# Performance work log

Hardware: AMD Instinct MI355X
Metric: run time of the kernel (lower is better)

Reference implementation:

```python
import jax, jax.numpy as jnp
import numpy as np

D_MODEL = 1024
NUM_HEADS = 16
D_HEAD = D_MODEL // NUM_HEADS
B, S = 4, 2048


def setup_inputs() -> dict:
    key = jax.random.key(0)
    ks = jax.random.split(key, 11)
    s = 1.0 / np.sqrt(D_MODEL)
    inp = {
        "query": jax.random.normal(ks[0], (B, S, D_MODEL), jnp.float32),
        "key": jax.random.normal(ks[1], (B, S, D_MODEL), jnp.float32),
        "value": jax.random.normal(ks[2], (B, S, D_MODEL), jnp.float32),
        "Wq": jax.random.uniform(ks[3], (D_MODEL, D_MODEL), jnp.float32, -s, s),
        "bq": jax.random.uniform(ks[4], (D_MODEL,), jnp.float32, -s, s),
        "Wk": jax.random.uniform(ks[5], (D_MODEL, D_MODEL), jnp.float32, -s, s),
        "bk": jax.random.uniform(ks[6], (D_MODEL,), jnp.float32, -s, s),
        "Wv": jax.random.uniform(ks[7], (D_MODEL, D_MODEL), jnp.float32, -s, s),
        "bv": jax.random.uniform(ks[8], (D_MODEL,), jnp.float32, -s, s),
        "Wo": jax.random.uniform(ks[9], (D_MODEL, D_MODEL), jnp.float32, -s, s),
        "bo": jax.random.uniform(ks[10], (D_MODEL,), jnp.float32, -s, s),
    }
    return inp


def reference(query, key, value, Wq, bq, Wk, bk, Wv, bv, Wo, bo):
    # Linear projections (torch Linear: x @ W.T + b)
    q = query @ Wq.T + bq  # [B,S,D]
    k = key @ Wk.T + bk
    v = value @ Wv.T + bv
    # split heads -> [B,H,S,Dh]
    def split(x):
        return x.reshape(B, S, NUM_HEADS, D_HEAD).transpose(0, 2, 1, 3)
    q, k, v = split(q), split(k), split(v)
    scale = 1.0 / np.sqrt(D_HEAD).astype(np.float32)
    scores = jnp.einsum('bhqd,bhkd->bhqk', q, k) * scale
    attn = jax.nn.softmax(scores, axis=-1)  # dropout is identity in eval
    ctx = jnp.einsum('bhqk,bhkd->bhqd', attn, v)
    ctx = ctx.transpose(0, 2, 1, 3).reshape(B, S, D_MODEL)
    return ctx @ Wo.T + bo
```

## Files before the change

kernel.cpp:

```cpp
#include <hip/hip_runtime.h>
#include <hip/hip_bf16.h>

typedef __bf16 bf16;
typedef bf16 bf16x8 __attribute__((ext_vector_type(8)));
typedef float f32x4 __attribute__((ext_vector_type(4)));
typedef float f32x16 __attribute__((ext_vector_type(16)));
typedef unsigned int u32x2 __attribute__((ext_vector_type(2)));
typedef unsigned int u32x4 __attribute__((ext_vector_type(4)));

#define B_  4
#define S_  2048
#define DM  1024
#define NH  16
#define DH  64

#define QSCALE 0.18033688011112042f


__device__ __forceinline__ void async_copy16(const void* g, void* lds) {
    __builtin_amdgcn_global_load_lds(
        (const __attribute__((address_space(1))) void*)g,
        (__attribute__((address_space(3))) void*)lds,
        16, 0, 0);
}

__device__ __forceinline__ bf16x8 read_frag(const char* lds, int row, int kbyte) {
    int off = row * 128 + (kbyte ^ ((row & 7) << 4));
    return *(const bf16x8*)(lds + off);
}

template<int ROWS>
__device__ __forceinline__ void stage_g2l(const bf16* g, int gs, char* lds) {
    int t = threadIdx.x;
#pragma unroll
    for (int i = 0; i < ROWS * 8 / 256; ++i) {
        int c = i * 256 + t;
        int r = c >> 3;
        int s = (c & 7) ^ (r & 7);
        async_copy16(g + r * gs + s * 8, lds + c * 16);
    }
}

__device__ __forceinline__ unsigned cvt_pk(float lo, float hi) {
    unsigned r;
    asm("v_cvt_pk_bf16_f32 %0, %1, %2" : "=v"(r) : "v"(lo), "v"(hi));
    return r;
}

__device__ __forceinline__ u32x2 pl32swap(unsigned a, unsigned b) {
    return __builtin_amdgcn_permlane32_swap(a, b, false, false);
}


__device__ __forceinline__ void cvt_body(const float* __restrict__ s, bf16* __restrict__ d, int n8) {
    for (int i = blockIdx.x * 256 + threadIdx.x; i < n8; i += gridDim.x * 256) {
        f32x4 v0 = *(const f32x4*)(s + (long)i * 8);
        f32x4 v1 = *(const f32x4*)(s + (long)i * 8 + 4);
        bf16x8 r;
#pragma unroll
        for (int j = 0; j < 4; ++j) { r[j] = (bf16)v0[j]; r[j + 4] = (bf16)v1[j]; }
        *(bf16x8*)(d + (long)i * 8) = r;
    }
}

__global__ __launch_bounds__(256) void cvt_x(
    const float* __restrict__ a, const float* __restrict__ b, const float* __restrict__ c,
    bf16* __restrict__ oa, bf16* __restrict__ ob, bf16* __restrict__ oc)
{
    int z = blockIdx.y;
    cvt_body(z == 0 ? a : z == 1 ? b : c, z == 0 ? oa : z == 1 ? ob : oc, B_ * S_ * DM / 8);
}

__global__ __launch_bounds__(256) void cvt_w(
    const float* __restrict__ a, const float* __restrict__ b,
    const float* __restrict__ c, const float* __restrict__ d,
    bf16* __restrict__ oa, bf16* __restrict__ ob, bf16* __restrict__ oc, bf16* __restrict__ od)
{
    int z = blockIdx.y;
    cvt_body(z == 0 ? a : z == 1 ? b : z == 2 ? c : d,
             z == 0 ? oa : z == 1 ? ob : z == 2 ? oc : od, DM * DM / 8);
}


__device__ __forceinline__ void gemm_main(
    const bf16* __restrict__ A, const bf16* __restrict__ Wt,
    char* As, char* Bs, int m0, int n0, int lane, int wm, int wn, f32x4 (&acc)[4][4])
{
#pragma unroll
    for (int i = 0; i < 4; ++i)
#pragma unroll
        for (int j = 0; j < 4; ++j) acc[i][j] = f32x4{0.f, 0.f, 0.f, 0.f};

    for (int k0 = 0; k0 < DM; k0 += 64) {
        __syncthreads();
        stage_g2l<128>(A + (long)m0 * DM + k0, DM, As);
        stage_g2l<128>(Wt + (long)n0 * DM + k0, DM, Bs);
        __syncthreads();
#pragma unroll
        for (int ks = 0; ks < 2; ++ks) {
            int kb = ks * 64 + (lane >> 4) * 16;
            bf16x8 af[4], bfr[4];
#pragma unroll
            for (int f = 0; f < 4; ++f) af[f]  = read_frag(As, wm + f * 16 + (lane & 15), kb);
#pragma unroll
            for (int f = 0; f < 4; ++f) bfr[f] = read_frag(Bs, wn + f * 16 + (lane & 15), kb);
#pragma unroll
            for (int mf = 0; mf < 4; ++mf)
#pragma unroll
                for (int nf = 0; nf < 4; ++nf)
                    acc[mf][nf] = __builtin_amdgcn_mfma_f32_16x16x32_bf16(
                        af[mf], bfr[nf], acc[mf][nf], 0, 0, 0);
        }
    }
}

__global__ __launch_bounds__(256) void qkv_gemm(
    const bf16* __restrict__ xq, const bf16* __restrict__ xk, const bf16* __restrict__ xv,
    const bf16* __restrict__ wq, const bf16* __restrict__ wk, const bf16* __restrict__ wv,
    const float* __restrict__ bq, const float* __restrict__ bk, const float* __restrict__ bv,
    bf16* __restrict__ qo, bf16* __restrict__ ko, bf16* __restrict__ vo)
{
    __shared__ alignas(128) char As[128 * 128];
    __shared__ alignas(128) char Bs[128 * 128];

    int z = blockIdx.z;
    const bf16* X     = (z == 0) ? xq : (z == 1) ? xk : xv;
    const bf16* W     = (z == 0) ? wq : (z == 1) ? wk : wv;
    const float* bias = (z == 0) ? bq : (z == 1) ? bk : bv;
    bf16* out         = (z == 0) ? qo : (z == 1) ? ko : vo;
    float scale       = (z == 0) ? QSCALE : 1.0f;
    bool  vt          = (z == 2);

    int m0 = blockIdx.y * 128, n0 = blockIdx.x * 128;
    int lane = threadIdx.x & 63, wid = threadIdx.x >> 6;
    int wm = (wid >> 1) * 64, wn = (wid & 1) * 64;

    f32x4 acc[4][4];
    gemm_main(X, W, As, Bs, m0, n0, lane, wm, wn, acc);

#pragma unroll
    for (int nf = 0; nf < 4; ++nf) {
        int j = n0 + wn + nf * 16 + (lane & 15);
        float bj = bias[j];
        int h = j >> 6, dh = j & 63;
#pragma unroll
        for (int mf = 0; mf < 4; ++mf) {
#pragma unroll
            for (int r = 0; r < 4; ++r) {
                int i = m0 + wm + mf * 16 + (lane >> 4) * 4 + r;
                float v = (acc[mf][nf][r] + bj) * scale;
                int b = i >> 11, s = i & 2047;
                long addr = vt ? ((long)((b * NH + h) * DH + dh)) * S_ + s
                               : ((long)((b * NH + h) * S_ + s)) * DH + dh;
                out[addr] = (bf16)v;
            }
        }
    }
}

__global__ __launch_bounds__(256) void out_gemm(
    const bf16* __restrict__ ctxb, const bf16* __restrict__ wo, const float* __restrict__ bo,
    float* __restrict__ out)
{
    __shared__ alignas(128) char As[128 * 128];
    __shared__ alignas(128) char Bs[128 * 128];

    int m0 = blockIdx.y * 128, n0 = blockIdx.x * 128;
    int lane = threadIdx.x & 63, wid = threadIdx.x >> 6;
    int wm = (wid >> 1) * 64, wn = (wid & 1) * 64;

    f32x4 acc[4][4];
    gemm_main(ctxb, wo, As, Bs, m0, n0, lane, wm, wn, acc);

#pragma unroll
    for (int nf = 0; nf < 4; ++nf) {
        int j = n0 + wn + nf * 16 + (lane & 15);
        float bj = bo[j];
#pragma unroll
        for (int mf = 0; mf < 4; ++mf)
#pragma unroll
            for (int r = 0; r < 4; ++r) {
                int i = m0 + wm + mf * 16 + (lane >> 4) * 4 + r;
                out[(long)i * DM + j] = acc[mf][nf][r] + bj;
            }
    }
}

__global__ __launch_bounds__(256) void attn_fwd(
    const bf16* __restrict__ qb, const bf16* __restrict__ kb, const bf16* __restrict__ vtb,
    bf16* __restrict__ ctx)
{
    __shared__ alignas(128) char Ks[2][64 * 128];
    __shared__ alignas(128) char Vs[2][64 * 128];

    int bid = blockIdx.x;
    int xcd = bid & 7, rest = bid >> 3;
    int qt = rest & 15, bh = xcd + 8 * (rest >> 4);

    int lane = threadIdx.x & 63, wid = threadIdx.x >> 6;
    int ln = lane & 31, h = lane >> 5;
    int q0w = qt * 128 + wid * 32;

    const bf16* qg = qb + (long)bh * S_ * DH;
    const bf16* kg = kb + (long)bh * S_ * DH;
    const bf16* vg = vtb + (long)bh * DH * S_;

    bf16x8 qf[4];
#pragma unroll
    for (int s = 0; s < 4; ++s)
        qf[s] = *(const bf16x8*)(qg + (long)(q0w + ln) * DH + s * 16 + h * 8);

    const bf16x8 onea = __builtin_bit_cast(bf16x8,
        u32x4{0x3F803F80u, 0x3F803F80u, 0x3F803F80u, 0x3F803F80u});

    f32x16 o[2];
#pragma unroll
    for (int t = 0; t < 2; ++t)
#pragma unroll
        for (int r = 0; r < 16; ++r) o[t][r] = 0.f;
    f32x16 lacc;
#pragma unroll
    for (int r = 0; r < 16; ++r) lacc[r] = 0.f;

    stage_g2l<64>(kg, DH, Ks[0]);
    stage_g2l<64>(vg, S_, Vs[0]);
    __syncthreads();

    int cur = 0;
    for (int kt2 = 0; kt2 < S_ / 64; ++kt2) {
        f32x16 acc[2];
#pragma unroll
        for (int t = 0; t < 2; ++t)
#pragma unroll
            for (int r = 0; r < 16; ++r) acc[t][r] = 0.f;
        __builtin_amdgcn_s_setprio(1);
#pragma unroll
        for (int t = 0; t < 2; ++t)
#pragma unroll
            for (int s = 0; s < 4; ++s) {
                bf16x8 ka = read_frag(Ks[cur], 32 * t + ln, 32 * s + 16 * h);
                acc[t] = __builtin_amdgcn_mfma_f32_32x32x16_bf16(ka, qf[s], acc[t], 0, 0, 0);
            }
        __builtin_amdgcn_s_setprio(0);

        if (kt2 + 1 < S_ / 64) {
            stage_g2l<64>(kg + (long)(kt2 + 1) * 64 * DH, DH, Ks[cur ^ 1]);
            stage_g2l<64>(vg + (kt2 + 1) * 64, S_, Vs[cur ^ 1]);
        }

#pragma unroll
        for (int t = 0; t < 2; ++t)
#pragma unroll
            for (int r = 0; r < 16; ++r)
                acc[t][r] = __builtin_amdgcn_exp2f(acc[t][r]);

        unsigned pf[4][4];
#pragma unroll
        for (int t = 0; t < 2; ++t)
#pragma unroll
            for (int hf = 0; hf < 2; ++hf) {
                int rb = 8 * hf;
                unsigned a0 = cvt_pk(acc[t][rb + 0], acc[t][rb + 1]);
                unsigned s0 = cvt_pk(acc[t][rb + 4], acc[t][rb + 5]);
                unsigned a1 = cvt_pk(acc[t][rb + 2], acc[t][rb + 3]);
                unsigned s1 = cvt_pk(acc[t][rb + 6], acc[t][rb + 7]);
                u32x2 r0 = pl32swap(a0, s0);
                u32x2 r1 = pl32swap(a1, s1);
                int kt = 2 * t + hf;
                pf[kt][0] = r0.x; pf[kt][2] = r0.y;
                pf[kt][1] = r1.x; pf[kt][3] = r1.y;
            }

        __builtin_amdgcn_s_setprio(1);
#pragma unroll
        for (int kt = 0; kt < 4; ++kt) {
            bf16x8 pb = __builtin_bit_cast(bf16x8,
                u32x4{pf[kt][0], pf[kt][1], pf[kt][2], pf[kt][3]});
            bf16x8 va0 = read_frag(Vs[cur], ln,      32 * kt + 16 * h);
            o[0] = __builtin_amdgcn_mfma_f32_32x32x16_bf16(va0, pb, o[0], 0, 0, 0);
            bf16x8 va1 = read_frag(Vs[cur], 32 + ln, 32 * kt + 16 * h);
            o[1] = __builtin_amdgcn_mfma_f32_32x32x16_bf16(va1, pb, o[1], 0, 0, 0);
            lacc = __builtin_amdgcn_mfma_f32_32x32x16_bf16(onea, pb, lacc, 0, 0, 0);
        }
        __builtin_amdgcn_s_setprio(0);

        __syncthreads();
        cur ^= 1;
    }

    int b = bh >> 4, head = bh & 15;
    float inv = 1.0f / lacc[0];
    int s = q0w + ln;
    bf16* base = ctx + ((long)(b * S_ + s)) * DM + head * DH;
#pragma unroll
    for (int dt = 0; dt < 2; ++dt)
#pragma unroll
        for (int c = 0; c < 4; ++c) {
            int d0 = 32 * dt + 8 * c + 4 * h;
            u32x2 st;
            st.x = cvt_pk(o[dt][4 * c + 0] * inv, o[dt][4 * c + 1] * inv);
            st.y = cvt_pk(o[dt][4 * c + 2] * inv, o[dt][4 * c + 3] * inv);
            *(u32x2*)(base + d0) = st;
        }
}

extern "C" void kernel_launch(void* const* d_in, const int* in_sizes, int n_in,
                              void* d_out, int out_size, void* d_ws, size_t ws_size,
                              hipStream_t stream) {
    const float* query = (const float*)d_in[0];
    const float* key   = (const float*)d_in[1];
    const float* value = (const float*)d_in[2];
    const float* Wq = (const float*)d_in[3];
    const float* bq = (const float*)d_in[4];
    const float* Wk = (const float*)d_in[5];
    const float* bk = (const float*)d_in[6];
    const float* Wv = (const float*)d_in[7];
    const float* bv = (const float*)d_in[8];
    const float* Wo = (const float*)d_in[9];
    const float* bo = (const float*)d_in[10];
    float* out = (float*)d_out;

    char* ws = (char*)d_ws;
    const long MB = 1ll << 20;
    bf16* qb   = (bf16*)(ws + 0 * MB);
    bf16* kb   = (bf16*)(ws + 16 * MB);
    bf16* vtb  = (bf16*)(ws + 32 * MB);
    bf16* xqb  = (bf16*)(ws + 48 * MB);
    bf16* xkb  = (bf16*)(ws + 64 * MB);
    bf16* xvb  = (bf16*)(ws + 80 * MB);
    bf16* wqb  = (bf16*)(ws + 96 * MB);
    bf16* wkb  = (bf16*)(ws + 98 * MB);
    bf16* wvb  = (bf16*)(ws + 100 * MB);
    bf16* wob  = (bf16*)(ws + 102 * MB);
    bf16* ctxb = xqb;

    dim3 blk(256);
    cvt_x<<<dim3(2048, 3), blk, 0, stream>>>(query, key, value, xqb, xkb, xvb);
    cvt_w<<<dim3(512, 4), blk, 0, stream>>>(Wq, Wk, Wv, Wo, wqb, wkb, wvb, wob);
    qkv_gemm<<<dim3(8, 64, 3), blk, 0, stream>>>(xqb, xkb, xvb, wqb, wkb, wvb,
                                                 bq, bk, bv, qb, kb, vtb);
    attn_fwd<<<dim3(1024), blk, 0, stream>>>(qb, kb, vtb, ctxb);
    out_gemm<<<dim3(8, 64), blk, 0, stream>>>(ctxb, wob, bo, out);
}
```

Before: 237.5 us.

## Replace projection GEMMs with 256x256 8-wave pipelined double-buffered kernels

Rewrites the QKV and output projection GEMMs to use 256x256 tiles with 512 threads and 128KB of LDS. Global-to-LDS async loads for the next K slabs are interleaved with MFMA phases under explicit vmcnt waits and barriers. The aim is to hide load latency and raise data reuse per tile, replacing the previous sync-load-compute loop. In exchange the grid shrinks considerably (128 blocks for the output GEMM), which may leave CUs idle, and the large LDS footprint limits residency.

```diff
diff --git a/kernel.cpp b/kernel.cpp
--- a/kernel.cpp
+++ b/kernel.cpp
@@ -29,15 +29,15 @@
     return *(const bf16x8*)(lds + off);
 }
 
-template<int ROWS>
+template<int ROWS, int NT>
 __device__ __forceinline__ void stage_g2l(const bf16* g, int gs, char* lds) {
     int t = threadIdx.x;
 #pragma unroll
-    for (int i = 0; i < ROWS * 8 / 256; ++i) {
-        int c = i * 256 + t;
+    for (int i = 0; i < ROWS * 8 / NT; ++i) {
+        int c = i * NT + t;
         int r = c >> 3;
         int s = (c & 7) ^ (r & 7);
-        async_copy16(g + r * gs + s * 8, lds + c * 16);
+        async_copy16(g + (long)r * gs + s * 8, lds + c * 16);
     }
 }
 
@@ -82,46 +82,138 @@
 }
 
 
-__device__ __forceinline__ void gemm_main(
-    const bf16* __restrict__ A, const bf16* __restrict__ Wt,
-    char* As, char* Bs, int m0, int n0, int lane, int wm, int wn, f32x4 (&acc)[4][4])
-{
-#pragma unroll
-    for (int i = 0; i < 4; ++i)
-#pragma unroll
-        for (int j = 0; j < 4; ++j) acc[i][j] = f32x4{0.f, 0.f, 0.f, 0.f};
-
-    for (int k0 = 0; k0 < DM; k0 += 64) {
-        __syncthreads();
-        stage_g2l<128>(A + (long)m0 * DM + k0, DM, As);
-        stage_g2l<128>(Wt + (long)n0 * DM + k0, DM, Bs);
-        __syncthreads();
-#pragma unroll
-        for (int ks = 0; ks < 2; ++ks) {
-            int kb = ks * 64 + (lane >> 4) * 16;
-            bf16x8 af[4], bfr[4];
-#pragma unroll
-            for (int f = 0; f < 4; ++f) af[f]  = read_frag(As, wm + f * 16 + (lane & 15), kb);
-#pragma unroll
-            for (int f = 0; f < 4; ++f) bfr[f] = read_frag(Bs, wn + f * 16 + (lane & 15), kb);
+__device__ __forceinline__ void ph_read(const char* Ab, const char* Bb,
+        int qa, int qb, int wr, int wc, int lane,
+        bf16x8 (&af)[4][2], bf16x8 (&bfr)[2][2]) {
+#pragma unroll
+    for (int mf = 0; mf < 4; ++mf)
+#pragma unroll
+        for (int ks = 0; ks < 2; ++ks)
+            af[mf][ks] = read_frag(Ab, 128 * qa + 64 * wr + 16 * mf + (lane & 15),
+                                   ks * 64 + (lane >> 4) * 16);
+#pragma unroll
+    for (int nf = 0; nf < 2; ++nf)
+#pragma unroll
+        for (int ks = 0; ks < 2; ++ks)
+            bfr[nf][ks] = read_frag(Bb, 128 * qb + 32 * wc + 16 * nf + (lane & 15),
+                                    ks * 64 + (lane >> 4) * 16);
+}
+
+__device__ __forceinline__ void ph_mfma(bf16x8 (&af)[4][2], bf16x8 (&bfr)[2][2],
+                                        f32x4 (&acc)[4][2]) {
+    __builtin_amdgcn_s_barrier();
+    asm volatile("s_waitcnt lgkmcnt(0)" ::: "memory");
+    __builtin_amdgcn_sched_barrier(0);
+    __builtin_amdgcn_s_setprio(1);
+#pragma unroll
+    for (int mf = 0; mf < 4; ++mf)
+#pragma unroll
+        for (int nf = 0; nf < 2; ++nf)
+#pragma unroll
+            for (int ks = 0; ks < 2; ++ks)
+                acc[mf][nf] = __builtin_amdgcn_mfma_f32_16x16x32_bf16(
+                    af[mf][ks], bfr[nf][ks], acc[mf][nf], 0, 0, 0);
+    __builtin_amdgcn_s_setprio(0);
+    __builtin_amdgcn_s_barrier();
+}
+
+__device__ __forceinline__ void gemm8_core(
+    const bf16* __restrict__ Ap, const bf16* __restrict__ Bp,
+    char* lds, int wr, int wc, int lane, f32x4 (&acc)[2][2][4][2])
+{
+    const long K = 1024;
+    char* A0b = lds;
+    char* A1b = lds + 32768;
+    char* B0b = lds + 65536;
+    char* B1b = lds + 98304;
+
+#pragma unroll
+    for (int qa = 0; qa < 2; ++qa)
+#pragma unroll
+        for (int qb = 0; qb < 2; ++qb)
 #pragma unroll
             for (int mf = 0; mf < 4; ++mf)
 #pragma unroll
-                for (int nf = 0; nf < 4; ++nf)
-                    acc[mf][nf] = __builtin_amdgcn_mfma_f32_16x16x32_bf16(
-                        af[mf], bfr[nf], acc[mf][nf], 0, 0, 0);
-        }
+                for (int nf = 0; nf < 2; ++nf)
+                    acc[qa][qb][mf][nf] = f32x4{0.f, 0.f, 0.f, 0.f};
+
+    stage_g2l<128, 512>(Ap,            K, A0b);
+    stage_g2l<128, 512>(Ap + 128 * K,  K, A0b + 16384);
+    stage_g2l<128, 512>(Bp,            K, B0b);
+    stage_g2l<128, 512>(Bp + 128 * K,  K, B0b + 16384);
+    stage_g2l<128, 512>(Ap + 64,       K, A1b);
+    stage_g2l<128, 512>(Bp + 64,       K, B1b);
+    asm volatile("s_waitcnt vmcnt(4)" ::: "memory");
+    __builtin_amdgcn_s_barrier();
+
+    bf16x8 af[4][2], bfr[2][2];
+    for (int it = 0; it < 7; ++it) {
+        const bf16* Aod = Ap + 64 * (2 * it + 1);
+        const bf16* Bod = Bp + 64 * (2 * it + 1);
+        const bf16* Aev = Ap + 64 * (2 * it + 2);
+        const bf16* Bev = Bp + 64 * (2 * it + 2);
+        const bf16* Ao2 = Ap + 64 * (2 * it + 3);
+        const bf16* Bo2 = Bp + 64 * (2 * it + 3);
+
+        ph_read(A0b, B0b, 0, 0, wr, wc, lane, af, bfr);
+        stage_g2l<128, 512>(Aod + 128 * K, K, A1b + 16384);
+        stage_g2l<128, 512>(Bod + 128 * K, K, B1b + 16384);
+        ph_mfma(af, bfr, acc[0][0]);
+        ph_read(A0b, B0b, 0, 1, wr, wc, lane, af, bfr);
+        ph_mfma(af, bfr, acc[0][1]);
+        ph_read(A0b, B0b, 1, 0, wr, wc, lane, af, bfr);
+        stage_g2l<128, 512>(Aev, K, A0b);
+        ph_mfma(af, bfr, acc[1][0]);
+        ph_read(A0b, B0b, 1, 1, wr, wc, lane, af, bfr);
+        stage_g2l<128, 512>(Bev, K, B0b);
+        asm volatile("s_waitcnt vmcnt(4)" ::: "memory");
+        ph_mfma(af, bfr, acc[1][1]);
+        ph_read(A1b, B1b, 0, 0, wr, wc, lane, af, bfr);
+        stage_g2l<128, 512>(Aev + 128 * K, K, A0b + 16384);
+        stage_g2l<128, 512>(Bev + 128 * K, K, B0b + 16384);
+        ph_mfma(af, bfr, acc[0][0]);
+        ph_read(A1b, B1b, 0, 1, wr, wc, lane, af, bfr);
+        ph_mfma(af, bfr, acc[0][1]);
+        ph_read(A1b, B1b, 1, 0, wr, wc, lane, af, bfr);
+        stage_g2l<128, 512>(Ao2, K, A1b);
+        ph_mfma(af, bfr, acc[1][0]);
+        ph_read(A1b, B1b, 1, 1, wr, wc, lane, af, bfr);
+        stage_g2l<128, 512>(Bo2, K, B1b);
+        asm volatile("s_waitcnt vmcnt(4)" ::: "memory");
+        ph_mfma(af, bfr, acc[1][1]);
     }
-}
-
-__global__ __launch_bounds__(256) void qkv_gemm(
+    {
+        const bf16* Aod = Ap + 64 * 15;
+        const bf16* Bod = Bp + 64 * 15;
+        ph_read(A0b, B0b, 0, 0, wr, wc, lane, af, bfr);
+        stage_g2l<128, 512>(Aod + 128 * K, K, A1b + 16384);
+        stage_g2l<128, 512>(Bod + 128 * K, K, B1b + 16384);
+        ph_mfma(af, bfr, acc[0][0]);
+        ph_read(A0b, B0b, 0, 1, wr, wc, lane, af, bfr);
+        ph_mfma(af, bfr, acc[0][1]);
+        ph_read(A0b, B0b, 1, 0, wr, wc, lane, af, bfr);
+        ph_mfma(af, bfr, acc[1][0]);
+        ph_read(A0b, B0b, 1, 1, wr, wc, lane, af, bfr);
+        asm volatile("s_waitcnt vmcnt(0)" ::: "memory");
+        ph_mfma(af, bfr, acc[1][1]);
+        ph_read(A1b, B1b, 0, 0, wr, wc, lane, af, bfr);
+        ph_mfma(af, bfr, acc[0][0]);
+        ph_read(A1b, B1b, 0, 1, wr, wc, lane, af, bfr);
+        ph_mfma(af, bfr, acc[0][1]);
+        ph_read(A1b, B1b, 1, 0, wr, wc, lane, af, bfr);
+        ph_mfma(af, bfr, acc[1][0]);
+        ph_read(A1b, B1b, 1, 1, wr, wc, lane, af, bfr);
+        ph_mfma(af, bfr, acc[1][1]);
+    }
+}
+
+__global__ __launch_bounds__(512, 2) void qkv_gemm8(
     const bf16* __restrict__ xq, const bf16* __restrict__ xk, const bf16* __restrict__ xv,
     const bf16* __restrict__ wq, const bf16* __restrict__ wk, const bf16* __restrict__ wv,
     const float* __restrict__ bq, const float* __restrict__ bk, const float* __restrict__ bv,
     bf16* __restrict__ qo, bf16* __restrict__ ko, bf16* __restrict__ vo)
 {
-    __shared__ alignas(128) char As[128 * 128];
-    __shared__ alignas(128) char Bs[128 * 128];
+    __shared__ alignas(128) char lds[131072];
 
     int z = blockIdx.z;
     const bf16* X     = (z == 0) ? xq : (z == 1) ? xk : xv;
@@ -131,59 +223,65 @@
     float scale       = (z == 0) ? QSCALE : 1.0f;
     bool  vt          = (z == 2);
 
-    int m0 = blockIdx.y * 128, n0 = blockIdx.x * 128;
+    int m0 = blockIdx.y * 256, n0 = blockIdx.x * 256;
     int lane = threadIdx.x & 63, wid = threadIdx.x >> 6;
-    int wm = (wid >> 1) * 64, wn = (wid & 1) * 64;
-
-    f32x4 acc[4][4];
-    gemm_main(X, W, As, Bs, m0, n0, lane, wm, wn, acc);
-
-#pragma unroll
-    for (int nf = 0; nf < 4; ++nf) {
-        int j = n0 + wn + nf * 16 + (lane & 15);
-        float bj = bias[j];
-        int h = j >> 6, dh = j & 63;
-#pragma unroll
-        for (int mf = 0; mf < 4; ++mf) {
-#pragma unroll
-            for (int r = 0; r < 4; ++r) {
-                int i = m0 + wm + mf * 16 + (lane >> 4) * 4 + r;
-                float v = (acc[mf][nf][r] + bj) * scale;
-                int b = i >> 11, s = i & 2047;
-                long addr = vt ? ((long)((b * NH + h) * DH + dh)) * S_ + s
-                               : ((long)((b * NH + h) * S_ + s)) * DH + dh;
-                out[addr] = (bf16)v;
+    int wr = wid >> 2, wc = wid & 3;
+
+    f32x4 acc[2][2][4][2];
+    gemm8_core(X + (long)m0 * DM, W + (long)n0 * DM, lds, wr, wc, lane, acc);
+
+#pragma unroll
+    for (int qa = 0; qa < 2; ++qa)
+#pragma unroll
+        for (int qb = 0; qb < 2; ++qb)
+#pragma unroll
+            for (int nf = 0; nf < 2; ++nf) {
+                int j = n0 + 128 * qb + 32 * wc + 16 * nf + (lane & 15);
+                float bj = bias[j];
+                int h = j >> 6, dh = j & 63;
+#pragma unroll
+                for (int mf = 0; mf < 4; ++mf)
+#pragma unroll
+                    for (int r = 0; r < 4; ++r) {
+                        int i = m0 + 128 * qa + 64 * wr + 16 * mf + (lane >> 4) * 4 + r;
+                        float v = (acc[qa][qb][mf][nf][r] + bj) * scale;
+                        int b = i >> 11, s = i & 2047;
+                        long addr = vt ? ((long)((b * NH + h) * DH + dh)) * S_ + s
+                                       : ((long)((b * NH + h) * S_ + s)) * DH + dh;
+                        out[addr] = (bf16)v;
+                    }
             }
-        }
-    }
-}
-
-__global__ __launch_bounds__(256) void out_gemm(
+}
+
+__global__ __launch_bounds__(512, 2) void out_gemm8(
     const bf16* __restrict__ ctxb, const bf16* __restrict__ wo, const float* __restrict__ bo,
     float* __restrict__ out)
 {
-    __shared__ alignas(128) char As[128 * 128];
-    __shared__ alignas(128) char Bs[128 * 128];
-
-    int m0 = blockIdx.y * 128, n0 = blockIdx.x * 128;
+    __shared__ alignas(128) char lds[131072];
+
+    int m0 = blockIdx.y * 256, n0 = blockIdx.x * 256;
     int lane = threadIdx.x & 63, wid = threadIdx.x >> 6;
-    int wm = (wid >> 1) * 64, wn = (wid & 1) * 64;
-
-    f32x4 acc[4][4];
-    gemm_main(ctxb, wo, As, Bs, m0, n0, lane, wm, wn, acc);
-
-#pragma unroll
-    for (int nf = 0; nf < 4; ++nf) {
-        int j = n0 + wn + nf * 16 + (lane & 15);
-        float bj = bo[j];
-#pragma unroll
-        for (int mf = 0; mf < 4; ++mf)
-#pragma unroll
-            for (int r = 0; r < 4; ++r) {
-                int i = m0 + wm + mf * 16 + (lane >> 4) * 4 + r;
-                out[(long)i * DM + j] = acc[mf][nf][r] + bj;
+    int wr = wid >> 2, wc = wid & 3;
+
+    f32x4 acc[2][2][4][2];
+    gemm8_core(ctxb + (long)m0 * DM, wo + (long)n0 * DM, lds, wr, wc, lane, acc);
+
+#pragma unroll
+    for (int qa = 0; qa < 2; ++qa)
+#pragma unroll
+        for (int qb = 0; qb < 2; ++qb)
+#pragma unroll
+            for (int nf = 0; nf < 2; ++nf) {
+                int j = n0 + 128 * qb + 32 * wc + 16 * nf + (lane & 15);
+                float bj = bo[j];
+#pragma unroll
+                for (int mf = 0; mf < 4; ++mf)
+#pragma unroll
+                    for (int r = 0; r < 4; ++r) {
+                        int i = m0 + 128 * qa + 64 * wr + 16 * mf + (lane >> 4) * 4 + r;
+                        out[(long)i * DM + j] = acc[qa][qb][mf][nf][r] + bj;
+                    }
             }
-    }
 }
 
 __global__ __launch_bounds__(256) void attn_fwd(
@@ -222,8 +320,8 @@
 #pragma unroll
     for (int r = 0; r < 16; ++r) lacc[r] = 0.f;
 
-    stage_g2l<64>(kg, DH, Ks[0]);
-    stage_g2l<64>(vg, S_, Vs[0]);
+    stage_g2l<64, 256>(kg, DH, Ks[0]);
+    stage_g2l<64, 256>(vg, S_, Vs[0]);
     __syncthreads();
 
     int cur = 0;
@@ -244,8 +342,8 @@
         __builtin_amdgcn_s_setprio(0);
 
         if (kt2 + 1 < S_ / 64) {
-            stage_g2l<64>(kg + (long)(kt2 + 1) * 64 * DH, DH, Ks[cur ^ 1]);
-            stage_g2l<64>(vg + (kt2 + 1) * 64, S_, Vs[cur ^ 1]);
+            stage_g2l<64, 256>(kg + (long)(kt2 + 1) * 64 * DH, DH, Ks[cur ^ 1]);
+            stage_g2l<64, 256>(vg + (kt2 + 1) * 64, S_, Vs[cur ^ 1]);
         }
 
 #pragma unroll
@@ -337,8 +435,8 @@
     dim3 blk(256);
     cvt_x<<<dim3(2048, 3), blk, 0, stream>>>(query, key, value, xqb, xkb, xvb);
     cvt_w<<<dim3(512, 4), blk, 0, stream>>>(Wq, Wk, Wv, Wo, wqb, wkb, wvb, wob);
-    qkv_gemm<<<dim3(8, 64, 3), blk, 0, stream>>>(xqb, xkb, xvb, wqb, wkb, wvb,
-                                                 bq, bk, bv, qb, kb, vtb);
+    qkv_gemm8<<<dim3(4, 32, 3), dim3(512), 0, stream>>>(xqb, xkb, xvb, wqb, wkb, wvb,
+                                                        bq, bk, bv, qb, kb, vtb);
     attn_fwd<<<dim3(1024), blk, 0, stream>>>(qb, kb, vtb, ctxb);
-    out_gemm<<<dim3(8, 64), blk, 0, stream>>>(ctxb, wob, bo, out);
-}
+    out_gemm8<<<dim3(4, 32), dim3(512), 0, stream>>>(ctxb, wob, bo, out);
+}
```

After: 255.5 us. +7.6%, slower.

## Fuse fp32-to-bf16 activation conversion into QKV GEMM A-tile loading

Applied to the files above, without the earlier changes.

Drops the separate cvt_x pass and has qkv_gemm read fp32 query/key/value directly into registers, convert them to bf16 and write the swizzled A tile into LDS. The next tile's fp32 loads are prefetched into registers while the weights are staged asynchronously, using manual waitcnt and barrier control. This removes a full write and re-read of the bf16 activation copies plus one kernel launch. In exchange, each GEMM block reads the fp32 A rows eight times (once per N-tile), so A traffic through cache doubles in bytes, and register pressure rises.

```diff
diff --git a/kernel.cpp b/kernel.cpp
--- a/kernel.cpp
+++ b/kernel.cpp
@@ -29,15 +29,15 @@
     return *(const bf16x8*)(lds + off);
 }
 
-template<int ROWS>
+template<int ROWS, int NT>
 __device__ __forceinline__ void stage_g2l(const bf16* g, int gs, char* lds) {
     int t = threadIdx.x;
 #pragma unroll
-    for (int i = 0; i < ROWS * 8 / 256; ++i) {
-        int c = i * 256 + t;
+    for (int i = 0; i < ROWS * 8 / NT; ++i) {
+        int c = i * NT + t;
         int r = c >> 3;
         int s = (c & 7) ^ (r & 7);
-        async_copy16(g + r * gs + s * 8, lds + c * 16);
+        async_copy16(g + (long)r * gs + s * 8, lds + c * 16);
     }
 }
 
@@ -61,14 +61,6 @@
         for (int j = 0; j < 4; ++j) { r[j] = (bf16)v0[j]; r[j + 4] = (bf16)v1[j]; }
         *(bf16x8*)(d + (long)i * 8) = r;
     }
-}
-
-__global__ __launch_bounds__(256) void cvt_x(
-    const float* __restrict__ a, const float* __restrict__ b, const float* __restrict__ c,
-    bf16* __restrict__ oa, bf16* __restrict__ ob, bf16* __restrict__ oc)
-{
-    int z = blockIdx.y;
-    cvt_body(z == 0 ? a : z == 1 ? b : c, z == 0 ? oa : z == 1 ? ob : oc, B_ * S_ * DM / 8);
 }
 
 __global__ __launch_bounds__(256) void cvt_w(
@@ -81,41 +73,8 @@
              z == 0 ? oa : z == 1 ? ob : z == 2 ? oc : od, DM * DM / 8);
 }
 
-
-__device__ __forceinline__ void gemm_main(
-    const bf16* __restrict__ A, const bf16* __restrict__ Wt,
-    char* As, char* Bs, int m0, int n0, int lane, int wm, int wn, f32x4 (&acc)[4][4])
-{
-#pragma unroll
-    for (int i = 0; i < 4; ++i)
-#pragma unroll
-        for (int j = 0; j < 4; ++j) acc[i][j] = f32x4{0.f, 0.f, 0.f, 0.f};
-
-    for (int k0 = 0; k0 < DM; k0 += 64) {
-        __syncthreads();
-        stage_g2l<128>(A + (long)m0 * DM + k0, DM, As);
-        stage_g2l<128>(Wt + (long)n0 * DM + k0, DM, Bs);
-        __syncthreads();
-#pragma unroll
-        for (int ks = 0; ks < 2; ++ks) {
-            int kb = ks * 64 + (lane >> 4) * 16;
-            bf16x8 af[4], bfr[4];
-#pragma unroll
-            for (int f = 0; f < 4; ++f) af[f]  = read_frag(As, wm + f * 16 + (lane & 15), kb);
-#pragma unroll
-            for (int f = 0; f < 4; ++f) bfr[f] = read_frag(Bs, wn + f * 16 + (lane & 15), kb);
-#pragma unroll
-            for (int mf = 0; mf < 4; ++mf)
-#pragma unroll
-                for (int nf = 0; nf < 4; ++nf)
-                    acc[mf][nf] = __builtin_amdgcn_mfma_f32_16x16x32_bf16(
-                        af[mf], bfr[nf], acc[mf][nf], 0, 0, 0);
-        }
-    }
-}
-
 __global__ __launch_bounds__(256) void qkv_gemm(
-    const bf16* __restrict__ xq, const bf16* __restrict__ xk, const bf16* __restrict__ xv,
+    const float* __restrict__ xq, const float* __restrict__ xk, const float* __restrict__ xv,
     const bf16* __restrict__ wq, const bf16* __restrict__ wk, const bf16* __restrict__ wv,
     const float* __restrict__ bq, const float* __restrict__ bk, const float* __restrict__ bv,
     bf16* __restrict__ qo, bf16* __restrict__ ko, bf16* __restrict__ vo)
@@ -124,7 +83,7 @@
     __shared__ alignas(128) char Bs[128 * 128];
 
     int z = blockIdx.z;
-    const bf16* X     = (z == 0) ? xq : (z == 1) ? xk : xv;
+    const float* X    = (z == 0) ? xq : (z == 1) ? xk : xv;
     const bf16* W     = (z == 0) ? wq : (z == 1) ? wk : wv;
     const float* bias = (z == 0) ? bq : (z == 1) ? bk : bv;
     bf16* out         = (z == 0) ? qo : (z == 1) ? ko : vo;
@@ -135,8 +94,61 @@
     int lane = threadIdx.x & 63, wid = threadIdx.x >> 6;
     int wm = (wid >> 1) * 64, wn = (wid & 1) * 64;
 
+    int t = threadIdx.x;
+    int arow = t >> 1, ac0 = (t & 1) * 32;
+    const float* Xb = X + (long)(m0 + arow) * DM + ac0;
+
     f32x4 acc[4][4];
-    gemm_main(X, W, As, Bs, m0, n0, lane, wm, wn, acc);
+#pragma unroll
+    for (int i = 0; i < 4; ++i)
+#pragma unroll
+        for (int j = 0; j < 4; ++j) acc[i][j] = f32x4{0.f, 0.f, 0.f, 0.f};
+
+    f32x4 av[8];
+#pragma unroll
+    for (int j = 0; j < 8; ++j) av[j] = *(const f32x4*)(Xb + 4 * j);
+
+    for (int k0 = 0; k0 < DM; k0 += 64) {
+        __builtin_amdgcn_s_barrier();
+        asm volatile("s_waitcnt vmcnt(0)" ::: "memory");
+#pragma unroll
+        for (int j = 0; j < 4; ++j) {
+            u32x4 w;
+            w.x = cvt_pk(av[2 * j][0], av[2 * j][1]);
+            w.y = cvt_pk(av[2 * j][2], av[2 * j][3]);
+            w.z = cvt_pk(av[2 * j + 1][0], av[2 * j + 1][1]);
+            w.w = cvt_pk(av[2 * j + 1][2], av[2 * j + 1][3]);
+            int kb = (ac0 * 2 + 16 * j) ^ ((arow & 7) << 4);
+            *(u32x4*)(As + arow * 128 + kb) = w;
+        }
+        stage_g2l<128, 256>(W + (long)n0 * DM + k0, DM, Bs);
+        __builtin_amdgcn_sched_barrier(0);
+        if (k0 + 64 < DM) {
+#pragma unroll
+            for (int j = 0; j < 8; ++j) av[j] = *(const f32x4*)(Xb + k0 + 64 + 4 * j);
+            asm volatile("s_waitcnt vmcnt(8)" ::: "memory");
+        } else {
+            asm volatile("s_waitcnt vmcnt(0)" ::: "memory");
+        }
+        asm volatile("s_waitcnt lgkmcnt(0)" ::: "memory");
+        __builtin_amdgcn_s_barrier();
+
+#pragma unroll
+        for (int ks = 0; ks < 2; ++ks) {
+            int kb = ks * 64 + (lane >> 4) * 16;
+            bf16x8 af[4], bfr[4];
+#pragma unroll
+            for (int f = 0; f < 4; ++f) af[f]  = read_frag(As, wm + f * 16 + (lane & 15), kb);
+#pragma unroll
+            for (int f = 0; f < 4; ++f) bfr[f] = read_frag(Bs, wn + f * 16 + (lane & 15), kb);
+#pragma unroll
+            for (int mf = 0; mf < 4; ++mf)
+#pragma unroll
+                for (int nf = 0; nf < 4; ++nf)
+                    acc[mf][nf] = __builtin_amdgcn_mfma_f32_16x16x32_bf16(
+                        af[mf], bfr[nf], acc[mf][nf], 0, 0, 0);
+        }
+    }
 
 #pragma unroll
     for (int nf = 0; nf < 4; ++nf) {
@@ -170,7 +182,32 @@
     int wm = (wid >> 1) * 64, wn = (wid & 1) * 64;
 
     f32x4 acc[4][4];
-    gemm_main(ctxb, wo, As, Bs, m0, n0, lane, wm, wn, acc);
+#pragma unroll
+    for (int i = 0; i < 4; ++i)
+#pragma unroll
+        for (int j = 0; j < 4; ++j) acc[i][j] = f32x4{0.f, 0.f, 0.f, 0.f};
+
+    for (int k0 = 0; k0 < DM; k0 += 64) {
+        __syncthreads();
+        stage_g2l<128, 256>(ctxb + (long)m0 * DM + k0, DM, As);
+        stage_g2l<128, 256>(wo + (long)n0 * DM + k0, DM, Bs);
+        __syncthreads();
+#pragma unroll
+        for (int ks = 0; ks < 2; ++ks) {
+            int kb = ks * 64 + (lane >> 4) * 16;
+            bf16x8 af[4], bfr[4];
+#pragma unroll
+            for (int f = 0; f < 4; ++f) af[f]  = read_frag(As, wm + f * 16 + (lane & 15), kb);
+#pragma unroll
+            for (int f = 0; f < 4; ++f) bfr[f] = read_frag(Bs, wn + f * 16 + (lane & 15), kb);
+#pragma unroll
+            for (int mf = 0; mf < 4; ++mf)
+#pragma unroll
+                for (int nf = 0; nf < 4; ++nf)
+                    acc[mf][nf] = __builtin_amdgcn_mfma_f32_16x16x32_bf16(
+                        af[mf], bfr[nf], acc[mf][nf], 0, 0, 0);
+        }
+    }
 
 #pragma unroll
     for (int nf = 0; nf < 4; ++nf) {
@@ -222,8 +259,8 @@
 #pragma unroll
     for (int r = 0; r < 16; ++r) lacc[r] = 0.f;
 
-    stage_g2l<64>(kg, DH, Ks[0]);
-    stage_g2l<64>(vg, S_, Vs[0]);
+    stage_g2l<64, 256>(kg, DH, Ks[0]);
+    stage_g2l<64, 256>(vg, S_, Vs[0]);
     __syncthreads();
 
     int cur = 0;
@@ -244,8 +281,8 @@
         __builtin_amdgcn_s_setprio(0);
 
         if (kt2 + 1 < S_ / 64) {
-            stage_g2l<64>(kg + (long)(kt2 + 1) * 64 * DH, DH, Ks[cur ^ 1]);
-            stage_g2l<64>(vg + (kt2 + 1) * 64, S_, Vs[cur ^ 1]);
+            stage_g2l<64, 256>(kg + (long)(kt2 + 1) * 64 * DH, DH, Ks[cur ^ 1]);
+            stage_g2l<64, 256>(vg + (kt2 + 1) * 64, S_, Vs[cur ^ 1]);
         }
 
 #pragma unroll
@@ -325,19 +362,15 @@
     bf16* qb   = (bf16*)(ws + 0 * MB);
     bf16* kb   = (bf16*)(ws + 16 * MB);
     bf16* vtb  = (bf16*)(ws + 32 * MB);
-    bf16* xqb  = (bf16*)(ws + 48 * MB);
-    bf16* xkb  = (bf16*)(ws + 64 * MB);
-    bf16* xvb  = (bf16*)(ws + 80 * MB);
-    bf16* wqb  = (bf16*)(ws + 96 * MB);
-    bf16* wkb  = (bf16*)(ws + 98 * MB);
-    bf16* wvb  = (bf16*)(ws + 100 * MB);
-    bf16* wob  = (bf16*)(ws + 102 * MB);
-    bf16* ctxb = xqb;
+    bf16* ctxb = (bf16*)(ws + 48 * MB);
+    bf16* wqb  = (bf16*)(ws + 64 * MB);
+    bf16* wkb  = (bf16*)(ws + 66 * MB);
+    bf16* wvb  = (bf16*)(ws + 68 * MB);
+    bf16* wob  = (bf16*)(ws + 70 * MB);
 
     dim3 blk(256);
-    cvt_x<<<dim3(2048, 3), blk, 0, stream>>>(query, key, value, xqb, xkb, xvb);
     cvt_w<<<dim3(512, 4), blk, 0, stream>>>(Wq, Wk, Wv, Wo, wqb, wkb, wvb, wob);
-    qkv_gemm<<<dim3(8, 64, 3), blk, 0, stream>>>(xqb, xkb, xvb, wqb, wkb, wvb,
+    qkv_gemm<<<dim3(8, 64, 3), blk, 0, stream>>>(query, key, value, wqb, wkb, wvb,
                                                  bq, bk, bv, qb, kb, vtb);
     attn_fwd<<<dim3(1024), blk, 0, stream>>>(qb, kb, vtb, ctxb);
     out_gemm<<<dim3(8, 64), blk, 0, stream>>>(ctxb, wob, bo, out);
```

Measured after the change: 287.9 us. 21.2% more time.
